# Kernel optimization log

Measured on AMD Instinct MI355X. Metric: run time of the kernel, lower is better.

The kernel has to match this reference:

```python
import jax, jax.numpy as jnp
import numpy as np

T = 16  # fixed number of timesteps in the original module


def _lin(k, out_d, in_d):
    kw, kb = jax.random.split(k)
    s = 1.0 / np.sqrt(in_d)
    W = jax.random.uniform(kw, (out_d, in_d), minval=-s, maxval=s, dtype=jnp.float32)
    b = jax.random.uniform(kb, (out_d,), minval=-s, maxval=s, dtype=jnp.float32)
    return W, b


def setup_inputs() -> dict:
    key = jax.random.key(0)
    B = 8192
    k = jax.random.split(key, 16)
    x = jax.random.normal(k[0], (T, B, 64), dtype=jnp.float32)
    cue = jax.random.uniform(k[1], (B,), dtype=jnp.float32)
    hc1 = jnp.zeros((B, 256), jnp.float32)
    hc2 = jnp.zeros((B, 256), jnp.float32)
    hc3 = jnp.zeros((B, 256), jnp.float32)
    hc4 = jnp.zeros((B, 64), jnp.float32)
    W1i, b1i = _lin(k[2], 256, 64)
    W1h, b1h = _lin(k[3], 256, 256)
    Wf1, bf1 = _lin(k[4], 256, 64)
    W1o, b1o = _lin(k[5], 64, 256)
    W2i, b2i = _lin(k[6], 256, 64)
    W2h, b2h = _lin(k[7], 256, 256)
    Wf2, bf2 = _lin(k[8], 256, 64)
    W2o, b2o = _lin(k[9], 64, 256)
    W3i, b3i = _lin(k[10], 256, 130)
    W3h, b3h = _lin(k[11], 256, 256)
    W3o, b3o = _lin(k[12], 64, 256)
    Wfc, bfc = _lin(k[13], 2, 64)
    return dict(x=x, cue=cue, hc1=hc1, hc2=hc2, hc3=hc3, hc4=hc4,
                W1i=W1i, b1i=b1i, W1h=W1h, b1h=b1h, Wf1=Wf1, bf1=bf1, W1o=W1o, b1o=b1o,
                W2i=W2i, b2i=b2i, W2h=W2h, b2h=b2h, Wf2=Wf2, bf2=bf2, W2o=W2o, b2o=b2o,
                W3i=W3i, b3i=b3i, W3h=W3h, b3h=b3h, W3o=W3o, b3o=b3o, Wfc=Wfc, bfc=bfc)


def reference(x, cue, hc1, hc2, hc3, hc4,
              W1i, b1i, W1h, b1h, Wf1, bf1, W1o, b1o,
              W2i, b2i, W2h, b2h, Wf2, bf2, W2o, b2o,
              W3i, b3i, W3h, b3h, W3o, b3o, Wfc, bfc):
    B = x.shape[1]
    # cue row is the same at every timestep: [B, 2]
    cue_row = jnp.stack([cue * 10.0, 10.0 * jnp.abs(cue - 1.0)], axis=-1)

    def step(carry, xi):
        h1, h2, h3, h4 = carry
        # RNN stack 1 with feedback from hc4
        feed1 = h4 @ Wf1.T + bf1                                    # [B,256] (pre-tanh, stored)
        h1n = jnp.tanh(xi @ W1i.T + b1i + h1 @ W1h.T + b1h + jnp.tanh(feed1))
        out1 = jnp.tanh(h1n @ W1o.T + b1o)                           # [B,64]
        # RNN stack 2 with feedback from hc4
        feed2 = h4 @ Wf2.T + bf2
        h2n = jnp.tanh(xi @ W2i.T + b2i + h2 @ W2h.T + b2h + jnp.tanh(feed2))
        out2 = jnp.tanh(h2n @ W2o.T + b2o)                           # [B,64]
        # RNN stack 3 over concat(cue, out1, out2): [B,130]
        mid = jnp.concatenate([cue_row, out1, out2], axis=-1)
        h3n = jnp.tanh(mid @ W3i.T + b3i + h3 @ W3h.T + b3h)
        o = h3n @ W3o.T + b3o                                        # [B,64]; becomes next hc4
        of = jax.nn.relu(o)
        outf = of @ Wfc.T + bfc                                      # [B,2]
        return (h1n, h2n, h3n, o), (outf, out1, out2, feed1, feed2, of)

    (h1, h2, h3, h4), (oseq, o1, o2, f1, f2, ofa) = jax.lax.scan(
        step, (hc1, hc2, hc3, hc4), x)
    cue_arr = jnp.broadcast_to(cue_row[None, :, :], (T, B, 2))
    return (oseq, h1, h2, h3, h4, o1, o2, cue_arr, f1, f2, ofa)
```

## Files before the change

kernel.cpp:

```cpp
#include <hip/hip_runtime.h>

typedef unsigned short ushort_t;
typedef __attribute__((ext_vector_type(8))) __bf16 bf8v;
typedef __attribute__((ext_vector_type(4))) float f4v;
typedef __attribute__((ext_vector_type(4))) unsigned short us4v;

#define MFMA(a, b, c) __builtin_amdgcn_mfma_f32_16x16x32_bf16((a), (b), (c), 0, 0, 0)

#define B_TOT 8192
#define T_STEPS 16
#define M_TILE 32
#define LDH 264
#define LDS_SM 72
#define LDMID 168

#define OW1I 0
#define OW1H 16384
#define OWF1 81920
#define OW1O 98304
#define OW2I 114688
#define OW2H 131072
#define OWF2 196608
#define OW2O 212992
#define OW3I 229376
#define OW3H 270336
#define OW3O 335872
#define OWFC 352256
#define WS_TOTAL 353280

#define O_OSEQ 0
#define O_H1   262144
#define O_H2   2359296
#define O_H3   4456448
#define O_H4   6553600
#define O_O1   7077888
#define O_O2   15466496
#define O_CUE  23855104
#define O_F1   24117248
#define O_F2   57671680
#define O_OFA  91226112

__device__ __forceinline__ ushort_t f2bf(float f) {
  union { float f; unsigned u; } v; v.f = f;
  unsigned r = v.u + 0x7fffu + ((v.u >> 16) & 1u);
  return (ushort_t)(r >> 16);
}

__device__ __forceinline__ float fast_tanh(float x) {
  float e = __expf(2.0f * x);
  return 1.0f - 2.0f * __builtin_amdgcn_rcpf(e + 1.0f);
}

__device__ __forceinline__ void store_bf4(ushort_t* p, f4v v) {
  us4v q;
  q[0] = f2bf(v[0]); q[1] = f2bf(v[1]); q[2] = f2bf(v[2]); q[3] = f2bf(v[3]);
  *(us4v*)p = q;
}

__device__ __forceinline__ void nt_st4(float* p, f4v v) {
  __builtin_nontemporal_store(v, (f4v*)p);
}
__device__ __forceinline__ f4v nt_ld4(const float* p) {
  return __builtin_nontemporal_load((const f4v*)p);
}

__global__ void prep_kernel(const float* __restrict__ W1i, const float* __restrict__ W1h,
                            const float* __restrict__ Wf1, const float* __restrict__ W1o,
                            const float* __restrict__ W2i, const float* __restrict__ W2h,
                            const float* __restrict__ Wf2, const float* __restrict__ W2o,
                            const float* __restrict__ W3i, const float* __restrict__ W3h,
                            const float* __restrict__ W3o, const float* __restrict__ Wfc,
                            ushort_t* __restrict__ ws) {
  int i = blockIdx.x * blockDim.x + threadIdx.x;
  if (i >= WS_TOTAL) return;
  float v;
  if (i < OW1H)       v = W1i[i - OW1I];
  else if (i < OWF1)  v = W1h[i - OW1H];
  else if (i < OW1O)  v = Wf1[i - OWF1];
  else if (i < OW2I)  v = W1o[i - OW1O];
  else if (i < OW2H)  v = W2i[i - OW2I];
  else if (i < OWF2)  v = W2h[i - OW2H];
  else if (i < OW2O)  v = Wf2[i - OWF2];
  else if (i < OW3I)  v = W2o[i - OW2O];
  else if (i < OW3H) {
    int idx = i - OW3I; int j = idx / 160; int k = idx - j * 160;
    if (k < 64)       v = W3i[j * 130 + 2 + k];
    else if (k < 128) v = W3i[j * 130 + 66 + (k - 64)];
    else if (k < 130) v = W3i[j * 130 + (k - 128)];
    else              v = 0.0f;
  }
  else if (i < OW3O)  v = W3h[i - OW3H];
  else if (i < OWFC)  v = W3o[i - OW3O];
  else {
    int idx = i - OWFC; int j = idx / 64; int k = idx - j * 64;
    v = (j < 2) ? Wfc[j * 64 + k] : 0.0f;
  }
  ws[i] = f2bf(v);
}

__launch_bounds__(512, 2)
__global__ void rnn_kernel(const float* __restrict__ x, const float* __restrict__ cue,
                           const float* __restrict__ hc1, const float* __restrict__ hc2,
                           const float* __restrict__ hc3, const float* __restrict__ hc4,
                           const float* __restrict__ b1i, const float* __restrict__ b1h,
                           const float* __restrict__ bf1p, const float* __restrict__ b1o,
                           const float* __restrict__ b2i, const float* __restrict__ b2h,
                           const float* __restrict__ bf2p, const float* __restrict__ b2o,
                           const float* __restrict__ b3i, const float* __restrict__ b3h,
                           const float* __restrict__ b3o, const float* __restrict__ bfc,
                           const ushort_t* __restrict__ ws, float* __restrict__ out) {
  __shared__ ushort_t hs1[M_TILE * LDH], hs2[M_TILE * LDH], hs3[M_TILE * LDH];
  __shared__ ushort_t h4s[M_TILE * LDS_SM], xs[M_TILE * LDS_SM], ofs[M_TILE * LDS_SM];
  __shared__ ushort_t mid[M_TILE * LDMID];

  const int tid  = threadIdx.x;
  const int m0   = blockIdx.x * M_TILE;
  const int lane = tid & 63;
  const int w    = tid >> 6;
  const int ln   = lane & 15;
  const int quad = lane >> 4;
  const int koff = quad * 8;
  const int jt0  = 2 * w;

  for (int i = tid; i < M_TILE * 64; i += 512) {
    int m = i >> 6, j4 = (i & 63) * 4;
    store_bf4(&hs1[m * LDH + j4], nt_ld4(&hc1[(size_t)(m0 + m) * 256 + j4]));
    store_bf4(&hs2[m * LDH + j4], nt_ld4(&hc2[(size_t)(m0 + m) * 256 + j4]));
    store_bf4(&hs3[m * LDH + j4], nt_ld4(&hc3[(size_t)(m0 + m) * 256 + j4]));
  }
  {
    int m = tid >> 4, j4 = (tid & 15) * 4;
    store_bf4(&h4s[m * LDS_SM + j4], nt_ld4(&hc4[(size_t)(m0 + m) * 64 + j4]));
  }
  for (int i = tid; i < M_TILE * LDMID; i += 512) mid[i] = 0;
  {
    int t = tid >> 5, r = tid & 31;
    float c = cue[m0 + r];
    float* oc = out + O_CUE + ((size_t)t * B_TOT + m0 + r) * 2;
    __builtin_nontemporal_store(c * 10.0f, oc);
    __builtin_nontemporal_store(10.0f * fabsf(c - 1.0f), oc + 1);
  }
  __syncthreads();
  if (tid < M_TILE) {
    float c = cue[m0 + tid];
    mid[tid * LDMID + 128] = f2bf(c * 10.0f);
    mid[tid * LDMID + 129] = f2bf(10.0f * fabsf(c - 1.0f));
  }

  f4v bf1v[2], bf2v[2], bih1v[2], bih2v[2], b3shv[2];
#pragma unroll
  for (int i = 0; i < 2; ++i) {
    int j0 = (jt0 + i) * 16 + quad * 4;
#pragma unroll
    for (int r = 0; r < 4; ++r) {
      bf1v[i][r]  = bf1p[j0 + r];
      bf2v[i][r]  = bf2p[j0 + r];
      bih1v[i][r] = b1i[j0 + r] + b1h[j0 + r];
      bih2v[i][r] = b2i[j0 + r] + b2h[j0 + r];
      b3shv[i][r] = b3i[j0 + r] + b3h[j0 + r];
    }
  }
  const int jto3 = w & 3;
  const int j0o3 = jto3 * 16 + quad * 4;
  const bool isOut2 = (w >= 4);
  f4v bo3v;
#pragma unroll
  for (int r = 0; r < 4; ++r) bo3v[r] = isOut2 ? b2o[j0o3 + r] : b1o[j0o3 + r];
  const int jto5 = w >> 1;
  const int j0o5 = jto5 * 16 + quad * 4;
  const int mo5  = (w & 1) * 16 + ln;
  f4v b3ov;
#pragma unroll
  for (int r = 0; r < 4; ++r) b3ov[r] = b3o[j0o5 + r];
  const float bfcv0 = bfc[0], bfcv1 = bfc[1];

  __syncthreads();

  f4v acc1[2][2], acc2[2][2], acc3[2][2];

  for (int t = 0; t < T_STEPS; ++t) {
    {
      int r = tid >> 4, c4 = (tid & 15) * 4;
      const float* xp = x + ((size_t)t * B_TOT + m0 + r) * 64 + c4;
      store_bf4(&xs[r * LDS_SM + c4], nt_ld4(xp));
    }
    {
      f4v aF1[2][2], aF2[2][2];
#pragma unroll
      for (int i = 0; i < 2; ++i) {
#pragma unroll
        for (int mt = 0; mt < 2; ++mt) { aF1[i][mt] = bf1v[i]; aF2[i][mt] = bf2v[i]; }
      }
#pragma unroll
      for (int kk = 0; kk < 64; kk += 32) {
        bf8v b0 = *(const bf8v*)&h4s[ln * LDS_SM + kk + koff];
        bf8v b1 = *(const bf8v*)&h4s[(16 + ln) * LDS_SM + kk + koff];
#pragma unroll
        for (int i = 0; i < 2; ++i) {
          const int ar = ((jt0 + i) * 16 + ln) * 64 + kk + koff;
          bf8v a1 = *(const bf8v*)&ws[OWF1 + ar];
          bf8v a2 = *(const bf8v*)&ws[OWF2 + ar];
          aF1[i][0] = MFMA(a1, b0, aF1[i][0]);
          aF1[i][1] = MFMA(a1, b1, aF1[i][1]);
          aF2[i][0] = MFMA(a2, b0, aF2[i][0]);
          aF2[i][1] = MFMA(a2, b1, aF2[i][1]);
        }
      }
#pragma unroll
      for (int i = 0; i < 2; ++i) {
#pragma unroll
        for (int mt = 0; mt < 2; ++mt) {
          int j0 = (jt0 + i) * 16 + quad * 4;
          int m  = mt * 16 + ln;
          size_t rowoff = ((size_t)t * B_TOT + m0 + m) * 256 + j0;
          nt_st4(out + O_F1 + rowoff, aF1[i][mt]);
          nt_st4(out + O_F2 + rowoff, aF2[i][mt]);
          f4v t1, t2;
#pragma unroll
          for (int r = 0; r < 4; ++r) {
            t1[r] = fast_tanh(aF1[i][mt][r]) + bih1v[i][r];
            t2[r] = fast_tanh(aF2[i][mt][r]) + bih2v[i][r];
          }
          acc1[i][mt] = t1; acc2[i][mt] = t2; acc3[i][mt] = b3shv[i];
        }
      }
    }
    __syncthreads();

#pragma unroll
    for (int kk = 0; kk < 64; kk += 32) {
      bf8v b0 = *(const bf8v*)&xs[ln * LDS_SM + kk + koff];
      bf8v b1 = *(const bf8v*)&xs[(16 + ln) * LDS_SM + kk + koff];
#pragma unroll
      for (int i = 0; i < 2; ++i) {
        const int ar = ((jt0 + i) * 16 + ln) * 64 + kk + koff;
        bf8v a1 = *(const bf8v*)&ws[OW1I + ar];
        bf8v a2 = *(const bf8v*)&ws[OW2I + ar];
        acc1[i][0] = MFMA(a1, b0, acc1[i][0]);
        acc1[i][1] = MFMA(a1, b1, acc1[i][1]);
        acc2[i][0] = MFMA(a2, b0, acc2[i][0]);
        acc2[i][1] = MFMA(a2, b1, acc2[i][1]);
      }
    }
#pragma unroll
    for (int kk = 0; kk < 256; kk += 32) {
      bf8v q1a = *(const bf8v*)&hs1[ln * LDH + kk + koff];
      bf8v q1b = *(const bf8v*)&hs1[(16 + ln) * LDH + kk + koff];
      bf8v q2a = *(const bf8v*)&hs2[ln * LDH + kk + koff];
      bf8v q2b = *(const bf8v*)&hs2[(16 + ln) * LDH + kk + koff];
      bf8v q3a = *(const bf8v*)&hs3[ln * LDH + kk + koff];
      bf8v q3b = *(const bf8v*)&hs3[(16 + ln) * LDH + kk + koff];
#pragma unroll
      for (int i = 0; i < 2; ++i) {
        const int ar = ((jt0 + i) * 16 + ln) * 256 + kk + koff;
        bf8v a1 = *(const bf8v*)&ws[OW1H + ar];
        bf8v a2 = *(const bf8v*)&ws[OW2H + ar];
        bf8v a3 = *(const bf8v*)&ws[OW3H + ar];
        acc1[i][0] = MFMA(a1, q1a, acc1[i][0]);
        acc1[i][1] = MFMA(a1, q1b, acc1[i][1]);
        acc2[i][0] = MFMA(a2, q2a, acc2[i][0]);
        acc2[i][1] = MFMA(a2, q2b, acc2[i][1]);
        acc3[i][0] = MFMA(a3, q3a, acc3[i][0]);
        acc3[i][1] = MFMA(a3, q3b, acc3[i][1]);
      }
    }
#pragma unroll
    for (int i = 0; i < 2; ++i) {
#pragma unroll
      for (int mt = 0; mt < 2; ++mt) {
#pragma unroll
        for (int r = 0; r < 4; ++r) {
          acc1[i][mt][r] = fast_tanh(acc1[i][mt][r]);
          acc2[i][mt][r] = fast_tanh(acc2[i][mt][r]);
        }
      }
    }
    if (t == T_STEPS - 1) {
#pragma unroll
      for (int i = 0; i < 2; ++i) {
#pragma unroll
        for (int mt = 0; mt < 2; ++mt) {
          int j0 = (jt0 + i) * 16 + quad * 4;
          int m  = mt * 16 + ln;
          nt_st4(out + O_H1 + (size_t)(m0 + m) * 256 + j0, acc1[i][mt]);
          nt_st4(out + O_H2 + (size_t)(m0 + m) * 256 + j0, acc2[i][mt]);
        }
      }
    }
    __syncthreads();

#pragma unroll
    for (int i = 0; i < 2; ++i) {
#pragma unroll
      for (int mt = 0; mt < 2; ++mt) {
        int j0 = (jt0 + i) * 16 + quad * 4;
        int m  = mt * 16 + ln;
        store_bf4(&hs1[m * LDH + j0], acc1[i][mt]);
        store_bf4(&hs2[m * LDH + j0], acc2[i][mt]);
      }
    }
    __syncthreads();

    {
      const ushort_t* hsrc = isOut2 ? hs2 : hs1;
      const int wbase = isOut2 ? OW2O : OW1O;
      f4v aO[2];
      aO[0] = bo3v; aO[1] = bo3v;
#pragma unroll
      for (int kk = 0; kk < 256; kk += 32) {
        bf8v b0 = *(const bf8v*)&hsrc[ln * LDH + kk + koff];
        bf8v b1 = *(const bf8v*)&hsrc[(16 + ln) * LDH + kk + koff];
        bf8v a  = *(const bf8v*)&ws[wbase + (jto3 * 16 + ln) * 256 + kk + koff];
        aO[0] = MFMA(a, b0, aO[0]);
        aO[1] = MFMA(a, b1, aO[1]);
      }
#pragma unroll
      for (int mt = 0; mt < 2; ++mt) {
#pragma unroll
        for (int r = 0; r < 4; ++r) aO[mt][r] = fast_tanh(aO[mt][r]);
        int m = mt * 16 + ln;
        size_t ob = ((size_t)t * B_TOT + m0 + m) * 64 + j0o3;
        nt_st4(out + (isOut2 ? O_O2 : O_O1) + ob, aO[mt]);
        store_bf4(&mid[m * LDMID + (isOut2 ? 64 : 0) + j0o3], aO[mt]);
      }
    }
    __syncthreads();

#pragma unroll
    for (int kk = 0; kk < 160; kk += 32) {
      bf8v b0 = *(const bf8v*)&mid[ln * LDMID + kk + koff];
      bf8v b1 = *(const bf8v*)&mid[(16 + ln) * LDMID + kk + koff];
#pragma unroll
      for (int i = 0; i < 2; ++i) {
        bf8v a = *(const bf8v*)&ws[OW3I + ((jt0 + i) * 16 + ln) * 160 + kk + koff];
        acc3[i][0] = MFMA(a, b0, acc3[i][0]);
        acc3[i][1] = MFMA(a, b1, acc3[i][1]);
      }
    }
#pragma unroll
    for (int i = 0; i < 2; ++i) {
#pragma unroll
      for (int mt = 0; mt < 2; ++mt) {
#pragma unroll
        for (int r = 0; r < 4; ++r) acc3[i][mt][r] = fast_tanh(acc3[i][mt][r]);
        int j0 = (jt0 + i) * 16 + quad * 4;
        int m  = mt * 16 + ln;
        if (t == T_STEPS - 1)
          nt_st4(out + O_H3 + (size_t)(m0 + m) * 256 + j0, acc3[i][mt]);
        store_bf4(&hs3[m * LDH + j0], acc3[i][mt]);
      }
    }
    __syncthreads();

    {
      f4v aO = b3ov;
#pragma unroll
      for (int kk = 0; kk < 256; kk += 32) {
        bf8v b = *(const bf8v*)&hs3[mo5 * LDH + kk + koff];
        bf8v a = *(const bf8v*)&ws[OW3O + (jto5 * 16 + ln) * 256 + kk + koff];
        aO = MFMA(a, b, aO);
      }
      store_bf4(&h4s[mo5 * LDS_SM + j0o5], aO);
      if (t == T_STEPS - 1)
        nt_st4(out + O_H4 + (size_t)(m0 + mo5) * 64 + j0o5, aO);
      f4v rl;
#pragma unroll
      for (int r = 0; r < 4; ++r) rl[r] = fmaxf(aO[r], 0.0f);
      nt_st4(out + O_OFA + ((size_t)t * B_TOT + m0 + mo5) * 64 + j0o5, rl);
      store_bf4(&ofs[mo5 * LDS_SM + j0o5], rl);
    }
    __syncthreads();

    if (w < 2) {
      f4v aFc;
      aFc[0] = (quad == 0) ? bfcv0 : 0.0f;
      aFc[1] = (quad == 0) ? bfcv1 : 0.0f;
      aFc[2] = 0.0f; aFc[3] = 0.0f;
#pragma unroll
      for (int kk = 0; kk < 64; kk += 32) {
        bf8v b = *(const bf8v*)&ofs[(w * 16 + ln) * LDS_SM + kk + koff];
        bf8v a = *(const bf8v*)&ws[OWFC + ln * 64 + kk + koff];
        aFc = MFMA(a, b, aFc);
      }
      if (quad == 0) {
        float* po = out + O_OSEQ + ((size_t)t * B_TOT + m0 + w * 16 + ln) * 2;
        __builtin_nontemporal_store(aFc[0], po);
        __builtin_nontemporal_store(aFc[1], po + 1);
      }
    }
  }
}

extern "C" void kernel_launch(void* const* d_in, const int* in_sizes, int n_in,
                              void* d_out, int out_size, void* d_ws, size_t ws_size,
                              hipStream_t stream) {
  const float* x   = (const float*)d_in[0];
  const float* cue = (const float*)d_in[1];
  const float* hc1 = (const float*)d_in[2];
  const float* hc2 = (const float*)d_in[3];
  const float* hc3 = (const float*)d_in[4];
  const float* hc4 = (const float*)d_in[5];
  const float* W1i = (const float*)d_in[6];
  const float* b1i = (const float*)d_in[7];
  const float* W1h = (const float*)d_in[8];
  const float* b1h = (const float*)d_in[9];
  const float* Wf1 = (const float*)d_in[10];
  const float* bf1 = (const float*)d_in[11];
  const float* W1o = (const float*)d_in[12];
  const float* b1o = (const float*)d_in[13];
  const float* W2i = (const float*)d_in[14];
  const float* b2i = (const float*)d_in[15];
  const float* W2h = (const float*)d_in[16];
  const float* b2h = (const float*)d_in[17];
  const float* Wf2 = (const float*)d_in[18];
  const float* bf2 = (const float*)d_in[19];
  const float* W2o = (const float*)d_in[20];
  const float* b2o = (const float*)d_in[21];
  const float* W3i = (const float*)d_in[22];
  const float* b3i = (const float*)d_in[23];
  const float* W3h = (const float*)d_in[24];
  const float* b3h = (const float*)d_in[25];
  const float* W3o = (const float*)d_in[26];
  const float* b3o = (const float*)d_in[27];
  const float* Wfc = (const float*)d_in[28];
  const float* bfc = (const float*)d_in[29];

  ushort_t* ws = (ushort_t*)d_ws;
  float* out = (float*)d_out;

  prep_kernel<<<(WS_TOTAL + 511) / 512, 512, 0, stream>>>(
      W1i, W1h, Wf1, W1o, W2i, W2h, Wf2, W2o, W3i, W3h, W3o, Wfc, ws);

  rnn_kernel<<<B_TOT / M_TILE, 512, 0, stream>>>(
      x, cue, hc1, hc2, hc3, hc4,
      b1i, b1h, bf1, b1o, b2i, b2h, bf2, b2o, b3i, b3h, b3o, bfc,
      ws, out);
}
```

Baseline: 988.1 us.

## Prefetch weight fragments and next-step x into registers ahead of MFMA phases

Weight fragments for each matmul phase (feedback, input, recurrent, output, layer-3 input, layer-3 output, fc) are now loaded from global memory into registers one phase ahead, across barriers. The recurrent weights are double-buffered along the K loop. The next timestep's x tile is also loaded early. The goal is to hide global/L2 latency behind MFMA and barrier waits. The cost is much higher VGPR pressure, which may lower occupancy or cause spills.

```diff
diff --git a/kernel.cpp b/kernel.cpp
--- a/kernel.cpp
+++ b/kernel.cpp
@@ -177,12 +177,50 @@
   __syncthreads();
 
   f4v acc1[2][2], acc2[2][2], acc3[2][2];
+  bf8v pF[2][2][2];
+  bf8v pIH[2][2][2];
+  bf8v Ah[2][2][3];
+  bf8v pO[8];
+  bf8v pI3[5][2];
+  bf8v pO3[8];
+  bf8v pFc[2];
+  f4v  xv;
+
+#define LOAD_PF() do { \
+  _Pragma("unroll") for (int kq = 0; kq < 2; ++kq) \
+  _Pragma("unroll") for (int i = 0; i < 2; ++i) { \
+    const int ar = ((jt0 + i) * 16 + ln) * 64 + kq * 32 + koff; \
+    pF[kq][i][0] = *(const bf8v*)&ws[OWF1 + ar]; \
+    pF[kq][i][1] = *(const bf8v*)&ws[OWF2 + ar]; \
+  } } while (0)
+
+#define LOAD_XV(tt) do { \
+  int r_ = tid >> 4, c4_ = (tid & 15) * 4; \
+  xv = nt_ld4(x + ((size_t)(tt) * B_TOT + m0 + r_) * 64 + c4_); \
+  } while (0)
+
+  LOAD_PF();
+  LOAD_XV(0);
 
   for (int t = 0; t < T_STEPS; ++t) {
     {
       int r = tid >> 4, c4 = (tid & 15) * 4;
-      const float* xp = x + ((size_t)t * B_TOT + m0 + r) * 64 + c4;
-      store_bf4(&xs[r * LDS_SM + c4], nt_ld4(xp));
+      store_bf4(&xs[r * LDS_SM + c4], xv);
+    }
+#pragma unroll
+    for (int kq = 0; kq < 2; ++kq)
+#pragma unroll
+      for (int i = 0; i < 2; ++i) {
+        const int ar = ((jt0 + i) * 16 + ln) * 64 + kq * 32 + koff;
+        pIH[kq][i][0] = *(const bf8v*)&ws[OW1I + ar];
+        pIH[kq][i][1] = *(const bf8v*)&ws[OW2I + ar];
+      }
+#pragma unroll
+    for (int i = 0; i < 2; ++i) {
+      const int ar = ((jt0 + i) * 16 + ln) * 256 + koff;
+      Ah[0][i][0] = *(const bf8v*)&ws[OW1H + ar];
+      Ah[0][i][1] = *(const bf8v*)&ws[OW2H + ar];
+      Ah[0][i][2] = *(const bf8v*)&ws[OW3H + ar];
     }
     {
       f4v aF1[2][2], aF2[2][2];
@@ -192,18 +230,16 @@
         for (int mt = 0; mt < 2; ++mt) { aF1[i][mt] = bf1v[i]; aF2[i][mt] = bf2v[i]; }
       }
 #pragma unroll
-      for (int kk = 0; kk < 64; kk += 32) {
+      for (int kq = 0; kq < 2; ++kq) {
+        const int kk = kq * 32;
         bf8v b0 = *(const bf8v*)&h4s[ln * LDS_SM + kk + koff];
         bf8v b1 = *(const bf8v*)&h4s[(16 + ln) * LDS_SM + kk + koff];
 #pragma unroll
         for (int i = 0; i < 2; ++i) {
-          const int ar = ((jt0 + i) * 16 + ln) * 64 + kk + koff;
-          bf8v a1 = *(const bf8v*)&ws[OWF1 + ar];
-          bf8v a2 = *(const bf8v*)&ws[OWF2 + ar];
-          aF1[i][0] = MFMA(a1, b0, aF1[i][0]);
-          aF1[i][1] = MFMA(a1, b1, aF1[i][1]);
-          aF2[i][0] = MFMA(a2, b0, aF2[i][0]);
-          aF2[i][1] = MFMA(a2, b1, aF2[i][1]);
+          aF1[i][0] = MFMA(pF[kq][i][0], b0, aF1[i][0]);
+          aF1[i][1] = MFMA(pF[kq][i][0], b1, aF1[i][1]);
+          aF2[i][0] = MFMA(pF[kq][i][1], b0, aF2[i][0]);
+          aF2[i][1] = MFMA(pF[kq][i][1], b1, aF2[i][1]);
         }
       }
 #pragma unroll
@@ -228,22 +264,30 @@
     __syncthreads();
 
 #pragma unroll
-    for (int kk = 0; kk < 64; kk += 32) {
+    for (int kq = 0; kq < 2; ++kq) {
+      const int kk = kq * 32;
       bf8v b0 = *(const bf8v*)&xs[ln * LDS_SM + kk + koff];
       bf8v b1 = *(const bf8v*)&xs[(16 + ln) * LDS_SM + kk + koff];
 #pragma unroll
       for (int i = 0; i < 2; ++i) {
-        const int ar = ((jt0 + i) * 16 + ln) * 64 + kk + koff;
-        bf8v a1 = *(const bf8v*)&ws[OW1I + ar];
-        bf8v a2 = *(const bf8v*)&ws[OW2I + ar];
-        acc1[i][0] = MFMA(a1, b0, acc1[i][0]);
-        acc1[i][1] = MFMA(a1, b1, acc1[i][1]);
-        acc2[i][0] = MFMA(a2, b0, acc2[i][0]);
-        acc2[i][1] = MFMA(a2, b1, acc2[i][1]);
+        acc1[i][0] = MFMA(pIH[kq][i][0], b0, acc1[i][0]);
+        acc1[i][1] = MFMA(pIH[kq][i][0], b1, acc1[i][1]);
+        acc2[i][0] = MFMA(pIH[kq][i][1], b0, acc2[i][0]);
+        acc2[i][1] = MFMA(pIH[kq][i][1], b1, acc2[i][1]);
       }
     }
 #pragma unroll
     for (int kk = 0; kk < 256; kk += 32) {
+      const int cur = (kk >> 5) & 1;
+      if (kk < 224) {
+#pragma unroll
+        for (int i = 0; i < 2; ++i) {
+          const int ar = ((jt0 + i) * 16 + ln) * 256 + kk + 32 + koff;
+          Ah[cur ^ 1][i][0] = *(const bf8v*)&ws[OW1H + ar];
+          Ah[cur ^ 1][i][1] = *(const bf8v*)&ws[OW2H + ar];
+          Ah[cur ^ 1][i][2] = *(const bf8v*)&ws[OW3H + ar];
+        }
+      }
       bf8v q1a = *(const bf8v*)&hs1[ln * LDH + kk + koff];
       bf8v q1b = *(const bf8v*)&hs1[(16 + ln) * LDH + kk + koff];
       bf8v q2a = *(const bf8v*)&hs2[ln * LDH + kk + koff];
@@ -252,17 +296,19 @@
       bf8v q3b = *(const bf8v*)&hs3[(16 + ln) * LDH + kk + koff];
 #pragma unroll
       for (int i = 0; i < 2; ++i) {
-        const int ar = ((jt0 + i) * 16 + ln) * 256 + kk + koff;
-        bf8v a1 = *(const bf8v*)&ws[OW1H + ar];
-        bf8v a2 = *(const bf8v*)&ws[OW2H + ar];
-        bf8v a3 = *(const bf8v*)&ws[OW3H + ar];
-        acc1[i][0] = MFMA(a1, q1a, acc1[i][0]);
-        acc1[i][1] = MFMA(a1, q1b, acc1[i][1]);
-        acc2[i][0] = MFMA(a2, q2a, acc2[i][0]);
-        acc2[i][1] = MFMA(a2, q2b, acc2[i][1]);
-        acc3[i][0] = MFMA(a3, q3a, acc3[i][0]);
-        acc3[i][1] = MFMA(a3, q3b, acc3[i][1]);
-      }
+        acc1[i][0] = MFMA(Ah[cur][i][0], q1a, acc1[i][0]);
+        acc1[i][1] = MFMA(Ah[cur][i][0], q1b, acc1[i][1]);
+        acc2[i][0] = MFMA(Ah[cur][i][1], q2a, acc2[i][0]);
+        acc2[i][1] = MFMA(Ah[cur][i][1], q2b, acc2[i][1]);
+        acc3[i][0] = MFMA(Ah[cur][i][2], q3a, acc3[i][0]);
+        acc3[i][1] = MFMA(Ah[cur][i][2], q3b, acc3[i][1]);
+      }
+    }
+    {
+      const int wbase = isOut2 ? OW2O : OW1O;
+#pragma unroll
+      for (int kq = 0; kq < 8; ++kq)
+        pO[kq] = *(const bf8v*)&ws[wbase + (jto3 * 16 + ln) * 256 + kq * 32 + koff];
     }
 #pragma unroll
     for (int i = 0; i < 2; ++i) {
@@ -302,17 +348,22 @@
     __syncthreads();
 
     {
+#pragma unroll
+      for (int kq = 0; kq < 5; ++kq)
+#pragma unroll
+        for (int i = 0; i < 2; ++i)
+          pI3[kq][i] = *(const bf8v*)&ws[OW3I + ((jt0 + i) * 16 + ln) * 160 + kq * 32 + koff];
+
       const ushort_t* hsrc = isOut2 ? hs2 : hs1;
-      const int wbase = isOut2 ? OW2O : OW1O;
       f4v aO[2];
       aO[0] = bo3v; aO[1] = bo3v;
 #pragma unroll
-      for (int kk = 0; kk < 256; kk += 32) {
+      for (int kq = 0; kq < 8; ++kq) {
+        const int kk = kq * 32;
         bf8v b0 = *(const bf8v*)&hsrc[ln * LDH + kk + koff];
         bf8v b1 = *(const bf8v*)&hsrc[(16 + ln) * LDH + kk + koff];
-        bf8v a  = *(const bf8v*)&ws[wbase + (jto3 * 16 + ln) * 256 + kk + koff];
-        aO[0] = MFMA(a, b0, aO[0]);
-        aO[1] = MFMA(a, b1, aO[1]);
+        aO[0] = MFMA(pO[kq], b0, aO[0]);
+        aO[1] = MFMA(pO[kq], b1, aO[1]);
       }
 #pragma unroll
       for (int mt = 0; mt < 2; ++mt) {
@@ -327,14 +378,17 @@
     __syncthreads();
 
 #pragma unroll
-    for (int kk = 0; kk < 160; kk += 32) {
+    for (int kq = 0; kq < 8; ++kq)
+      pO3[kq] = *(const bf8v*)&ws[OW3O + (jto5 * 16 + ln) * 256 + kq * 32 + koff];
+#pragma unroll
+    for (int kq = 0; kq < 5; ++kq) {
+      const int kk = kq * 32;
       bf8v b0 = *(const bf8v*)&mid[ln * LDMID + kk + koff];
       bf8v b1 = *(const bf8v*)&mid[(16 + ln) * LDMID + kk + koff];
 #pragma unroll
       for (int i = 0; i < 2; ++i) {
-        bf8v a = *(const bf8v*)&ws[OW3I + ((jt0 + i) * 16 + ln) * 160 + kk + koff];
-        acc3[i][0] = MFMA(a, b0, acc3[i][0]);
-        acc3[i][1] = MFMA(a, b1, acc3[i][1]);
+        acc3[i][0] = MFMA(pI3[kq][i], b0, acc3[i][0]);
+        acc3[i][1] = MFMA(pI3[kq][i], b1, acc3[i][1]);
       }
     }
 #pragma unroll
@@ -352,13 +406,19 @@
     }
     __syncthreads();
 
+    LOAD_PF();
+    LOAD_XV(t + 1 < T_STEPS ? t + 1 : T_STEPS - 1);
+    if (w < 2) {
+      pFc[0] = *(const bf8v*)&ws[OWFC + ln * 64 + koff];
+      pFc[1] = *(const bf8v*)&ws[OWFC + ln * 64 + 32 + koff];
+    }
     {
       f4v aO = b3ov;
 #pragma unroll
-      for (int kk = 0; kk < 256; kk += 32) {
+      for (int kq = 0; kq < 8; ++kq) {
+        const int kk = kq * 32;
         bf8v b = *(const bf8v*)&hs3[mo5 * LDH + kk + koff];
-        bf8v a = *(const bf8v*)&ws[OW3O + (jto5 * 16 + ln) * 256 + kk + koff];
-        aO = MFMA(a, b, aO);
+        aO = MFMA(pO3[kq], b, aO);
       }
       store_bf4(&h4s[mo5 * LDS_SM + j0o5], aO);
       if (t == T_STEPS - 1)
@@ -377,10 +437,10 @@
       aFc[1] = (quad == 0) ? bfcv1 : 0.0f;
       aFc[2] = 0.0f; aFc[3] = 0.0f;
 #pragma unroll
-      for (int kk = 0; kk < 64; kk += 32) {
+      for (int kq = 0; kq < 2; ++kq) {
+        const int kk = kq * 32;
         bf8v b = *(const bf8v*)&ofs[(w * 16 + ln) * LDS_SM + kk + koff];
-        bf8v a = *(const bf8v*)&ws[OWFC + ln * 64 + kk + koff];
-        aFc = MFMA(a, b, aFc);
+        aFc = MFMA(pFc[kq], b, aFc);
       }
       if (quad == 0) {
         float* po = out + O_OSEQ + ((size_t)t * B_TOT + m0 + w * 16 + ln) * 2;
@@ -389,6 +449,8 @@
       }
     }
   }
+#undef LOAD_PF
+#undef LOAD_XV
 }
 
 extern "C" void kernel_launch(void* const* d_in, const int* in_sizes, int n_in,
```

Measured after the change: 968.2 us. -2.0%, faster.
